# Kernel optimization log

Measured on AMD Instinct MI355X. Metric: run time of the kernel, lower is better.

The kernel has to match this reference:

```python
import jax, jax.numpy as jnp
import numpy as np

EPS = 1e-12  # tf.contrib layer_norm default epsilon
FORGET_BIAS = 1.0  # tf LSTMCell default


def _layer_norm(x, gamma, beta):
    mu = jnp.mean(x, axis=-1, keepdims=True)
    var = jnp.mean(jnp.square(x - mu), axis=-1, keepdims=True)
    return (x - mu) * jax.lax.rsqrt(var + EPS) * gamma + beta


def setup_inputs() -> dict:
    key = jax.random.key(0)
    ks = jax.random.split(key, 16)
    B, T, OBS, ACT, H = 256, 512, 256, 64, 64
    N = B * T
    s = 0.05
    inp = {
        "obs": jax.random.normal(ks[0], (N, OBS), jnp.float32),
        "action": jax.random.normal(ks[1], (N, ACT), jnp.float32),
        "c0": jnp.zeros((B, H), jnp.float32),
        "h0": jnp.zeros((B, H), jnp.float32),
        "W_obs": jax.random.normal(ks[2], (OBS, H), jnp.float32) * s,
        "b_obs": jnp.zeros((H,), jnp.float32),
        "g1": jnp.ones((H,), jnp.float32),
        "beta1": jnp.zeros((H,), jnp.float32),
        "W_act": jax.random.normal(ks[3], (ACT, H), jnp.float32) * s,
        "b_act": jnp.zeros((H,), jnp.float32),
        "g2": jnp.ones((H,), jnp.float32),
        "beta2": jnp.zeros((H,), jnp.float32),
        "W_lstm": jax.random.normal(ks[4], (2 * H + H, 4 * H), jnp.float32) * s,
        "b_lstm": jnp.zeros((4 * H,), jnp.float32),
        "g3": jnp.ones((H,), jnp.float32),
        "beta3": jnp.zeros((H,), jnp.float32),
        "W_out": jax.random.uniform(ks[5], (H, 1), jnp.float32, -0.003, 0.003),
        "b_out": jnp.zeros((1,), jnp.float32),
        "batch_size": B,
        "step_size": T,
    }
    return inp


def reference(obs, action, c0, h0, W_obs, b_obs, g1, beta1, W_act, b_act, g2, beta2,
              W_lstm, b_lstm, g3, beta3, W_out, b_out, batch_size, step_size):
    H = 64
    # obs branch (output is overwritten below — faithful to source bug)
    x = jnp.maximum(_layer_norm(obs @ W_obs + b_obs, g1, beta1), 0.0)
    # action branch
    yd = action @ W_act + b_act
    x = _layer_norm(yd, g2, beta2)  # BUG in source: overwrites obs branch
    y = jnp.maximum(yd, 0.0)
    xy = jnp.concatenate([x, y], axis=-1)  # [B*T, 128]
    rnn_in = xy.reshape(batch_size, step_size, 2 * H).transpose(1, 0, 2)  # [T,B,128]

    def step(carry, x_t):
        c, h = carry
        z = jnp.concatenate([x_t, h], axis=-1) @ W_lstm + b_lstm  # [B,4H]
        i, j, f, o = jnp.split(z, 4, axis=-1)  # tf LSTMCell gate order
        c_new = c * jax.nn.sigmoid(f + FORGET_BIAS) + jax.nn.sigmoid(i) * jnp.tanh(j)
        h_new = jax.nn.sigmoid(o) * jnp.tanh(c_new)
        return (c_new, h_new), h_new

    (c_fin, h_fin), hs = jax.lax.scan(step, (c0, h0), rnn_in)  # hs: [T,B,H]
    out = hs.transpose(1, 0, 2).reshape(batch_size * step_size, H)
    out = _layer_norm(out, g3, beta3)
    q = out @ W_out + b_out  # [B*T, 1]
    return q, c_fin, h_fin
```

## Files before the change

### kernel.cpp

```cpp
#include <hip/hip_runtime.h>

#define HD 64
#define TT 512
#define BB 256
#define NROWS (BB * TT)

typedef __attribute__((ext_vector_type(8))) short short8_t;
typedef __attribute__((ext_vector_type(4))) float f32x4;

__device__ __forceinline__ float rl(float v, int k) {
  return __uint_as_float(__builtin_amdgcn_readlane(__float_as_uint(v), k));
}
__device__ __forceinline__ float wsum(float v) {
#pragma unroll
  for (int m = 32; m >= 1; m >>= 1) v += __shfl_xor(v, m, 64);
  return v;
}
__device__ __forceinline__ float sigmoidf_(float x) {
  return 1.0f / (1.0f + __expf(-x));
}
__device__ __forceinline__ float tanhf_(float x) {
  return 1.0f - 2.0f / (__expf(2.0f * x) + 1.0f);
}
__device__ __forceinline__ unsigned short f2bf(float f) {
  unsigned int u = __float_as_uint(f);
  u = (u + 0x7fffu + ((u >> 16) & 1u)) >> 16;
  return (unsigned short)u;
}
__device__ __forceinline__ float ldz(const float* p) { return *p; }
__device__ __forceinline__ float ldz(const unsigned short* p) {
  return __uint_as_float(((unsigned int)(*p)) << 16);
}
__device__ __forceinline__ void store8(float* p, float4 a, float4 b) {
  *(float4*)p = a;
  *(float4*)(p + 4) = b;
}
__device__ __forceinline__ void store8(unsigned short* p, float4 a, float4 b) {
  union { unsigned short us[8]; int4 v; } u;
  u.us[0] = f2bf(a.x); u.us[1] = f2bf(a.y); u.us[2] = f2bf(a.z); u.us[3] = f2bf(a.w);
  u.us[4] = f2bf(b.x); u.us[5] = f2bf(b.y); u.us[6] = f2bf(b.z); u.us[7] = f2bf(b.w);
  *(int4*)p = u.v;
}
__device__ __forceinline__ float4 fma4(float4 a, float s, float4 w) {
  a.x += s * w.x; a.y += s * w.y; a.z += s * w.z; a.w += s * w.w;
  return a;
}
__device__ __forceinline__ float4 add4(float4 a, float4 b) {
  a.x += b.x; a.y += b.y; a.z += b.z; a.w += b.w;
  return a;
}

template <typename ZT>
__global__ __launch_bounds__(256) void kA(const float* __restrict__ act,
                                          const float* __restrict__ Wact,
                                          const float* __restrict__ bact,
                                          const float* __restrict__ g2,
                                          const float* __restrict__ beta2,
                                          const float* __restrict__ Wl,
                                          const float* __restrict__ bl,
                                          ZT* __restrict__ Zx) {
  __shared__ float xy[64][128];
  const int tid = threadIdx.x;
  const int lane = tid & 63;
  const int wv = tid >> 6;
  const int r0blk = blockIdx.x * 64;

  float wreg[64];
#pragma unroll
  for (int k = 0; k < 64; ++k) wreg[k] = Wact[k * 64 + lane];
  const float ba = bact[lane], gg = g2[lane], bb = beta2[lane];

  for (int i = 0; i < 16; ++i) {
    const int r = i * 4 + wv;
    const int row = r0blk + r;
    const float a = act[row * 64 + lane];
    float yd = ba;
#pragma unroll
    for (int k = 0; k < 64; ++k) yd += rl(a, k) * wreg[k];
    const float mu = wsum(yd) * (1.0f / 64.0f);
    const float d = yd - mu;
    const float var = wsum(d * d) * (1.0f / 64.0f);
    const float x = d * rsqrtf(var + 1e-12f) * gg + bb;
    xy[r][lane] = x;
    xy[r][64 + lane] = fmaxf(yd, 0.0f);
  }
  __syncthreads();

  const int tc = tid & 31;
  const int tr = tid >> 5;
  const int c0 = tc * 8;
  float4 accA[8], accB[8];
#pragma unroll
  for (int r = 0; r < 8; ++r) {
    accA[r] = make_float4(0.f, 0.f, 0.f, 0.f);
    accB[r] = make_float4(0.f, 0.f, 0.f, 0.f);
  }
  for (int kk = 0; kk < 128; kk += 4) {
    float4 xv[8];
#pragma unroll
    for (int r = 0; r < 8; ++r) xv[r] = *(const float4*)&xy[tr * 8 + r][kk];
#pragma unroll
    for (int dk = 0; dk < 4; ++dk) {
      const float4 wa = *(const float4*)&Wl[(kk + dk) * 256 + c0];
      const float4 wb = *(const float4*)&Wl[(kk + dk) * 256 + c0 + 4];
#pragma unroll
      for (int r = 0; r < 8; ++r) {
        const float xr = (dk == 0) ? xv[r].x : (dk == 1) ? xv[r].y : (dk == 2) ? xv[r].z : xv[r].w;
        accA[r] = fma4(accA[r], xr, wa);
        accB[r] = fma4(accB[r], xr, wb);
      }
    }
  }
  const float4 bla = *(const float4*)&bl[c0];
  const float4 blb = *(const float4*)&bl[c0 + 4];
#pragma unroll
  for (int r = 0; r < 8; ++r) {
    const int row = r0blk + tr * 8 + r;
    store8(&Zx[(size_t)row * 256 + c0], add4(accA[r], bla), add4(accB[r], blb));
  }
}

template <typename ZT>
__global__ __launch_bounds__(64) void kB2(const ZT* __restrict__ Zx,
                                          const float* __restrict__ Wl,
                                          const float* __restrict__ c0p,
                                          const float* __restrict__ h0p,
                                          float* __restrict__ hs,
                                          float* __restrict__ cfin,
                                          float* __restrict__ hfin) {
  __shared__ __align__(16) unsigned short h_lds[64];
  const int l = threadIdx.x;
  const int b = blockIdx.x;
  const int grp = l >> 4;
  const int col = l & 15;

  short8_t wf0[16], wf1[16];
#pragma unroll
  for (int t16 = 0; t16 < 16; ++t16) {
    short8_t w0, w1;
#pragma unroll
    for (int j = 0; j < 8; ++j) {
      w0[j] = (short)f2bf(Wl[(128 + 0 + grp * 8 + j) * 256 + 16 * t16 + col]);
      w1[j] = (short)f2bf(Wl[(128 + 32 + grp * 8 + j) * 256 + 16 * t16 + col]);
    }
    wf0[t16] = w0;
    wf1[t16] = w1;
  }

  const f32x4 zc = {0.f, 0.f, 0.f, 0.f};

  float c = c0p[b * 64 + l];
  float h = h0p[b * 64 + l];

  const ZT* zrow = Zx + (size_t)b * TT * 256;
  float* hsrow = hs + (size_t)b * TT * 64;

#define LD4(PI, PJ, PF, PO, T)                       \
  PI = ldz(&zrow[(size_t)(T) * 256 + 0 + l]);        \
  PJ = ldz(&zrow[(size_t)(T) * 256 + 64 + l]);       \
  PF = ldz(&zrow[(size_t)(T) * 256 + 128 + l]);      \
  PO = ldz(&zrow[(size_t)(T) * 256 + 192 + l]);

  float pAi, pAj, pAf, pAo, pBi, pBj, pBf, pBo;
  float pCi, pCj, pCf, pCo, pDi, pDj, pDf, pDo;
  LD4(pAi, pAj, pAf, pAo, 0)
  LD4(pBi, pBj, pBf, pBo, 1)
  LD4(pCi, pCj, pCf, pCo, 2)
  LD4(pDi, pDj, pDf, pDo, 3)

#define STEP(PI, PJ, PF, PO, T)                                               \
  {                                                                           \
    h_lds[l] = f2bf(h);                                                       \
    asm volatile("s_waitcnt lgkmcnt(0)" ::: "memory");                        \
    const short8_t a0 = *(const short8_t*)&h_lds[grp * 8];                    \
    const short8_t a1 = *(const short8_t*)&h_lds[32 + grp * 8];               \
    f32x4 acc[16];                                                            \
    _Pragma("unroll") for (int t16 = 0; t16 < 16; ++t16) {                    \
      f32x4 tmp = __builtin_amdgcn_mfma_f32_16x16x32_bf16(a0, wf0[t16], zc, 0, 0, 0); \
      acc[t16] = __builtin_amdgcn_mfma_f32_16x16x32_bf16(a1, wf1[t16], tmp, 0, 0, 0); \
    }                                                                         \
    const float zi = (grp == 0 ? acc[0].x : grp == 1 ? acc[1].x : grp == 2 ? acc[2].x : acc[3].x) + PI;   \
    const float zj = (grp == 0 ? acc[4].x : grp == 1 ? acc[5].x : grp == 2 ? acc[6].x : acc[7].x) + PJ;   \
    const float zf = (grp == 0 ? acc[8].x : grp == 1 ? acc[9].x : grp == 2 ? acc[10].x : acc[11].x) + PF; \
    const float zo = (grp == 0 ? acc[12].x : grp == 1 ? acc[13].x : grp == 2 ? acc[14].x : acc[15].x) + PO; \
    int tn = (T) + 4;                                                         \
    if (tn > TT - 1) tn = TT - 1;                                             \
    LD4(PI, PJ, PF, PO, tn)                                                   \
    c = c * sigmoidf_(zf + 1.0f) + sigmoidf_(zi) * tanhf_(zj);                \
    h = sigmoidf_(zo) * tanhf_(c);                                            \
    hsrow[(size_t)(T) * 64 + l] = h;                                          \
  }

#pragma unroll 1
  for (int t = 0; t < TT; t += 4) {
    STEP(pAi, pAj, pAf, pAo, t)
    STEP(pBi, pBj, pBf, pBo, t + 1)
    STEP(pCi, pCj, pCf, pCo, t + 2)
    STEP(pDi, pDj, pDf, pDo, t + 3)
  }
#undef STEP
#undef LD4

  cfin[b * 64 + l] = c;
  hfin[b * 64 + l] = h;
}

__global__ __launch_bounds__(256) void kC(const float* __restrict__ hs,
                                          const float* __restrict__ g3,
                                          const float* __restrict__ beta3,
                                          const float* __restrict__ Wout,
                                          const float* __restrict__ bout,
                                          float* __restrict__ q) {
  const int lane = threadIdx.x & 63;
  const int wv = threadIdx.x >> 6;
  const float g = g3[lane], be = beta3[lane], wo = Wout[lane], bo = bout[0];
  for (int n = blockIdx.x * 4 + wv; n < NROWS; n += gridDim.x * 4) {
    const float v = hs[(size_t)n * 64 + lane];
    const float mu = wsum(v) * (1.0f / 64.0f);
    const float d = v - mu;
    const float var = wsum(d * d) * (1.0f / 64.0f);
    const float xn = d * rsqrtf(var + 1e-12f) * g + be;
    const float s = wsum(xn * wo);
    if (lane == 0) q[n] = s + bo;
  }
}

extern "C" void kernel_launch(void* const* d_in, const int* in_sizes, int n_in,
                              void* d_out, int out_size, void* d_ws, size_t ws_size,
                              hipStream_t stream) {
  const float* action = (const float*)d_in[1];
  const float* c0 = (const float*)d_in[2];
  const float* h0 = (const float*)d_in[3];
  const float* Wact = (const float*)d_in[8];
  const float* bact = (const float*)d_in[9];
  const float* g2 = (const float*)d_in[10];
  const float* b2 = (const float*)d_in[11];
  const float* Wl = (const float*)d_in[12];
  const float* bl = (const float*)d_in[13];
  const float* g3 = (const float*)d_in[14];
  const float* b3 = (const float*)d_in[15];
  const float* Wout = (const float*)d_in[16];
  const float* bout = (const float*)d_in[17];

  float* q = (float*)d_out;
  float* cfin = q + NROWS;
  float* hfin = cfin + BB * HD;

  const size_t zx32 = (size_t)NROWS * 256 * sizeof(float);
  const size_t zx16 = (size_t)NROWS * 256 * sizeof(unsigned short);
  const size_t hsb = (size_t)NROWS * 64 * sizeof(float);

  if (ws_size >= zx32 + hsb) {
    float* Zx = (float*)d_ws;
    float* hs = (float*)((char*)d_ws + zx32);
    kA<float><<<NROWS / 64, 256, 0, stream>>>(action, Wact, bact, g2, b2, Wl, bl, Zx);
    kB2<float><<<BB, 64, 0, stream>>>(Zx, Wl, c0, h0, hs, cfin, hfin);
    kC<<<2048, 256, 0, stream>>>(hs, g3, b3, Wout, bout, q);
  } else {
    unsigned short* Zx = (unsigned short*)d_ws;
    float* hs = (float*)((char*)d_ws + zx16);
    kA<unsigned short><<<NROWS / 64, 256, 0, stream>>>(action, Wact, bact, g2, b2, Wl, bl, Zx);
    kB2<unsigned short><<<BB, 64, 0, stream>>>(Zx, Wl, c0, h0, hs, cfin, hfin);
    kC<<<2048, 256, 0, stream>>>(hs, g3, b3, Wout, bout, q);
  }
}
```

Before: 505.3 us.

## Replace MFMA-based recurrent matvec with fp32 packed FMA using readlane broadcast

The LSTM recurrence kernel now keeps the hidden-to-gate weights as fp32 pairs in registers and computes each step's gates with packed FMAs. The hidden state is broadcast across lanes via readlane instead of staging bf16 h through LDS and running MFMA tiles. This removes the per-step LDS write/wait and the MFMA latency chain, and stops rounding h and weights to bf16. The cost is 256 weight registers per lane and 64 serial readlanes per step, which may pressure registers or lengthen the critical path.

```diff
diff --git a/kernel.cpp b/kernel.cpp
--- a/kernel.cpp
+++ b/kernel.cpp
@@ -5,8 +5,7 @@
 #define BB 256
 #define NROWS (BB * TT)
 
-typedef __attribute__((ext_vector_type(8))) short short8_t;
-typedef __attribute__((ext_vector_type(4))) float f32x4;
+typedef __attribute__((ext_vector_type(2))) float f32x2;
 
 __device__ __forceinline__ float rl(float v, int k) {
   return __uint_as_float(__builtin_amdgcn_readlane(__float_as_uint(v), k));
@@ -47,6 +46,11 @@
 }
 __device__ __forceinline__ float4 add4(float4 a, float4 b) {
   a.x += b.x; a.y += b.y; a.z += b.z; a.w += b.w;
+  return a;
+}
+__device__ __forceinline__ f32x2 pf2(f32x2 a, float s, f32x2 w) {
+  a.x += s * w.x;
+  a.y += s * w.y;
   return a;
 }
 
@@ -121,33 +125,26 @@
 }
 
 template <typename ZT>
-__global__ __launch_bounds__(64) void kB2(const ZT* __restrict__ Zx,
-                                          const float* __restrict__ Wl,
-                                          const float* __restrict__ c0p,
-                                          const float* __restrict__ h0p,
-                                          float* __restrict__ hs,
-                                          float* __restrict__ cfin,
-                                          float* __restrict__ hfin) {
-  __shared__ __align__(16) unsigned short h_lds[64];
+__global__ __launch_bounds__(64, 1) void kB3(const ZT* __restrict__ Zx,
+                                             const float* __restrict__ Wl,
+                                             const float* __restrict__ c0p,
+                                             const float* __restrict__ h0p,
+                                             float* __restrict__ hs,
+                                             float* __restrict__ cfin,
+                                             float* __restrict__ hfin) {
   const int l = threadIdx.x;
   const int b = blockIdx.x;
-  const int grp = l >> 4;
-  const int col = l & 15;
-
-  short8_t wf0[16], wf1[16];
-#pragma unroll
-  for (int t16 = 0; t16 < 16; ++t16) {
-    short8_t w0, w1;
-#pragma unroll
-    for (int j = 0; j < 8; ++j) {
-      w0[j] = (short)f2bf(Wl[(128 + 0 + grp * 8 + j) * 256 + 16 * t16 + col]);
-      w1[j] = (short)f2bf(Wl[(128 + 32 + grp * 8 + j) * 256 + 16 * t16 + col]);
-    }
-    wf0[t16] = w0;
-    wf1[t16] = w1;
-  }
-
-  const f32x4 zc = {0.f, 0.f, 0.f, 0.f};
+
+  f32x2 wij[64], wfo[64];
+#pragma unroll
+  for (int k = 0; k < 64; ++k) {
+    const float* wr = &Wl[(128 + k) * 256];
+    f32x2 a, bvec;
+    a.x = wr[l];       a.y = wr[64 + l];
+    bvec.x = wr[128 + l]; bvec.y = wr[192 + l];
+    wij[k] = a;
+    wfo[k] = bvec;
+  }
 
   float c = c0p[b * 64 + l];
   float h = h0p[b * 64 + l];
@@ -170,19 +167,21 @@
 
 #define STEP(PI, PJ, PF, PO, T)                                               \
   {                                                                           \
-    h_lds[l] = f2bf(h);                                                       \
-    asm volatile("s_waitcnt lgkmcnt(0)" ::: "memory");                        \
-    const short8_t a0 = *(const short8_t*)&h_lds[grp * 8];                    \
-    const short8_t a1 = *(const short8_t*)&h_lds[32 + grp * 8];               \
-    f32x4 acc[16];                                                            \
-    _Pragma("unroll") for (int t16 = 0; t16 < 16; ++t16) {                    \
-      f32x4 tmp = __builtin_amdgcn_mfma_f32_16x16x32_bf16(a0, wf0[t16], zc, 0, 0, 0); \
-      acc[t16] = __builtin_amdgcn_mfma_f32_16x16x32_bf16(a1, wf1[t16], tmp, 0, 0, 0); \
+    f32x2 a0, a1, a2, a3, f0, f1, f2, f3;                                     \
+    a0.x = PI; a0.y = PJ; f0.x = PF; f0.y = PO;                               \
+    a1 = a2 = a3 = f1 = f2 = f3 = (f32x2)(0.0f);                              \
+    _Pragma("unroll") for (int k = 0; k < 64; k += 4) {                       \
+      const float h0v = rl(h, k), h1v = rl(h, k + 1);                         \
+      const float h2v = rl(h, k + 2), h3v = rl(h, k + 3);                     \
+      a0 = pf2(a0, h0v, wij[k]);     f0 = pf2(f0, h0v, wfo[k]);               \
+      a1 = pf2(a1, h1v, wij[k + 1]); f1 = pf2(f1, h1v, wfo[k + 1]);           \
+      a2 = pf2(a2, h2v, wij[k + 2]); f2 = pf2(f2, h2v, wfo[k + 2]);           \
+      a3 = pf2(a3, h3v, wij[k + 3]); f3 = pf2(f3, h3v, wfo[k + 3]);           \
     }                                                                         \
-    const float zi = (grp == 0 ? acc[0].x : grp == 1 ? acc[1].x : grp == 2 ? acc[2].x : acc[3].x) + PI;   \
-    const float zj = (grp == 0 ? acc[4].x : grp == 1 ? acc[5].x : grp == 2 ? acc[6].x : acc[7].x) + PJ;   \
-    const float zf = (grp == 0 ? acc[8].x : grp == 1 ? acc[9].x : grp == 2 ? acc[10].x : acc[11].x) + PF; \
-    const float zo = (grp == 0 ? acc[12].x : grp == 1 ? acc[13].x : grp == 2 ? acc[14].x : acc[15].x) + PO; \
+    a0.x += a1.x; a0.y += a1.y; a2.x += a3.x; a2.y += a3.y;                   \
+    f0.x += f1.x; f0.y += f1.y; f2.x += f3.x; f2.y += f3.y;                   \
+    const float zi = a0.x + a2.x, zj = a0.y + a2.y;                           \
+    const float zf = f0.x + f2.x, zo = f0.y + f2.y;                           \
     int tn = (T) + 4;                                                         \
     if (tn > TT - 1) tn = TT - 1;                                             \
     LD4(PI, PJ, PF, PO, tn)                                                   \
@@ -254,13 +253,13 @@
     float* Zx = (float*)d_ws;
     float* hs = (float*)((char*)d_ws + zx32);
     kA<float><<<NROWS / 64, 256, 0, stream>>>(action, Wact, bact, g2, b2, Wl, bl, Zx);
-    kB2<float><<<BB, 64, 0, stream>>>(Zx, Wl, c0, h0, hs, cfin, hfin);
+    kB3<float><<<BB, 64, 0, stream>>>(Zx, Wl, c0, h0, hs, cfin, hfin);
     kC<<<2048, 256, 0, stream>>>(hs, g3, b3, Wout, bout, q);
   } else {
     unsigned short* Zx = (unsigned short*)d_ws;
     float* hs = (float*)((char*)d_ws + zx16);
     kA<unsigned short><<<NROWS / 64, 256, 0, stream>>>(action, Wact, bact, g2, b2, Wl, bl, Zx);
-    kB2<unsigned short><<<BB, 64, 0, stream>>>(Zx, Wl, c0, h0, hs, cfin, hfin);
+    kB3<unsigned short><<<BB, 64, 0, stream>>>(Zx, Wl, c0, h0, hs, cfin, hfin);
     kC<<<2048, 256, 0, stream>>>(hs, g3, b3, Wout, bout, q);
   }
 }
```

Result: slower. 1.477 ms (+192.2%).
